# Kernel optimization log

Hardware: AMD Instinct MI355X
Metric: run time of the kernel (lower is better)

## Reference

```python
import jax, jax.numpy as jnp
import numpy as np

N_NODES = 100000
N_EDGES = 600000
DIM = 128
N_BEHAVIORS = 4


def setup_inputs() -> dict:
    key = jax.random.key(0)
    ks = jax.random.split(key, 10)
    user = jax.random.randint(ks[0], (N_NODES,), 0, N_NODES, dtype=jnp.int32)
    item = jax.random.randint(ks[1], (N_NODES,), 0, N_NODES, dtype=jnp.int32)
    behavior = jax.random.randint(ks[2], (N_NODES,), 0, N_BEHAVIORS, dtype=jnp.int32)
    adj_rows = jax.random.randint(ks[3], (N_EDGES,), 0, N_NODES, dtype=jnp.int32)
    adj_cols = jax.random.randint(ks[4], (N_EDGES,), 0, N_NODES, dtype=jnp.int32)
    adj_vals = jax.random.uniform(ks[5], (N_EDGES,), dtype=jnp.float32)
    user_table = jax.random.normal(ks[6], (N_NODES, DIM), dtype=jnp.float32)
    item_table = jax.random.normal(ks[7], (N_NODES, DIM), dtype=jnp.float32)
    behavior_table = jax.random.normal(ks[8], (N_BEHAVIORS, DIM), dtype=jnp.float32)
    kw, kb = jax.random.split(ks[9])
    bound = 1.0 / np.sqrt(DIM)
    W = jax.random.uniform(kw, (DIM, DIM), minval=-bound, maxval=bound, dtype=jnp.float32)
    b = jax.random.uniform(kb, (DIM,), minval=-bound, maxval=bound, dtype=jnp.float32)
    return {"user": user, "item": item, "behavior": behavior,
            "adj_rows": adj_rows, "adj_cols": adj_cols, "adj_vals": adj_vals,
            "user_table": user_table, "item_table": item_table,
            "behavior_table": behavior_table, "W": W, "b": b}


def reference(user, item, behavior, adj_rows, adj_cols, adj_vals,
              user_table, item_table, behavior_table, W, b):
    # embedding sum: [N, D]
    x = user_table[user] + item_table[item] + behavior_table[behavior]
    # sparse adjacency matmul: out[r] = sum_e adj_vals[e] * x[cols[e]] for rows[e]==r
    msg = adj_vals[:, None] * x[adj_cols]                       # [E, D]
    agg = jax.ops.segment_sum(msg, adj_rows, num_segments=N_NODES)  # [N, D]
    # dense linear
    return agg @ W.T + b
```

## Files before the change

### kernel.cpp

```cpp
#include <hip/hip_runtime.h>

#define N_NODES 100000
#define N_EDGES 600000
#define DIM 128

#define N4 (N_NODES / 4)
#define SCAN_BLOCKS ((N_NODES + 1023) / 1024)

#define EMBED_B 6250
#define HIST_B  2344
#define WCONV_B 16
#define GEMM_B   782
#define BUCKET_B 2344
#define NTILES   1563

typedef __attribute__((ext_vector_type(8))) short bf16x8;
typedef __attribute__((ext_vector_type(4))) float f32x4;

__device__ __forceinline__ void fma4(float4& acc, float s, const float4 w) {
    acc.x = fmaf(s, w.x, acc.x);
    acc.y = fmaf(s, w.y, acc.y);
    acc.z = fmaf(s, w.z, acc.z);
    acc.w = fmaf(s, w.w, acc.w);
}

__device__ __forceinline__ unsigned short f2bf(float f) {
    union { float f; unsigned int u; } v; v.f = f;
    unsigned int r = v.u + 0x7fffu + ((v.u >> 16) & 1u);
    return (unsigned short)(r >> 16);
}

__device__ __forceinline__ float bf2f(unsigned short u) {
    union { unsigned int i; float f; } v;
    v.i = ((unsigned int)u) << 16;
    return v.f;
}

__global__ __launch_bounds__(256) void k1_kernel(
    const int* __restrict__ user, const int* __restrict__ item, const int* __restrict__ behavior,
    const float* __restrict__ ut, const float* __restrict__ itb, const float* __restrict__ bt,
    const int* __restrict__ rows, const float* __restrict__ W,
    unsigned short* __restrict__ x16, int* __restrict__ cnt, unsigned short* __restrict__ wfrag)
{
    int b = blockIdx.x;
    int t = threadIdx.x;
    if (b < EMBED_B) {
        int gid = b * 256 + t;
        int r = gid >> 4;
        int m = gid & 15;
        int u  = user[r];
        int iv = item[r];
        int bh = behavior[r];
        const float4* ut4 = (const float4*)ut;
        const float4* it4 = (const float4*)itb;
        const float4* bt4 = (const float4*)bt;
        float4 a0 = ut4[(size_t)u  * 32 + 2 * m];
        float4 a1 = ut4[(size_t)u  * 32 + 2 * m + 1];
        float4 c0 = it4[(size_t)iv * 32 + 2 * m];
        float4 c1 = it4[(size_t)iv * 32 + 2 * m + 1];
        float4 d0 = bt4[(size_t)bh * 32 + 2 * m];
        float4 d1 = bt4[(size_t)bh * 32 + 2 * m + 1];
        ushort4 o0, o1;
        o0.x = f2bf(a0.x + c0.x + d0.x);
        o0.y = f2bf(a0.y + c0.y + d0.y);
        o0.z = f2bf(a0.z + c0.z + d0.z);
        o0.w = f2bf(a0.w + c0.w + d0.w);
        o1.x = f2bf(a1.x + c1.x + d1.x);
        o1.y = f2bf(a1.y + c1.y + d1.y);
        o1.z = f2bf(a1.z + c1.z + d1.z);
        o1.w = f2bf(a1.w + c1.w + d1.w);
        unsigned short* xr = x16 + (size_t)r * DIM + 8 * m;
        *(ushort4*)xr       = o0;
        *(ushort4*)(xr + 4) = o1;
    } else if (b < EMBED_B + HIST_B) {
        int e = (b - EMBED_B) * 256 + t;
        if (e < N_EDGES) atomicAdd(&cnt[rows[e]], 1);
    } else {
        int c4 = (b - EMBED_B - HIST_B) * 256 + t;
        if (c4 < 128 * 128 / 4) {
            float4 wv = ((const float4*)W)[c4];
            int i  = c4 >> 5;
            int k0 = (c4 & 31) * 4;
            int slot = (i >> 4) * 4 + (k0 >> 5);
            int lane = ((k0 & 31) >> 3) * 16 + (i & 15);
            ushort4 o;
            o.x = f2bf(wv.x); o.y = f2bf(wv.y); o.z = f2bf(wv.z); o.w = f2bf(wv.w);
            *(ushort4*)&wfrag[slot * 512 + lane * 8 + (k0 & 7)] = o;
        }
    }
}

__global__ __launch_bounds__(256) void scan1_kernel(
    const int* __restrict__ cnt, int* __restrict__ off, int* __restrict__ bsum)
{
    __shared__ int s[256];
    int t = threadIdx.x;
    int b = blockIdx.x;
    int i4 = b * 256 + t;
    int4 c = {0, 0, 0, 0};
    if (i4 < N4) c = ((const int4*)cnt)[i4];
    int tsum = c.x + c.y + c.z + c.w;
    s[t] = tsum;
    __syncthreads();
    for (int d = 1; d < 256; d <<= 1) {
        int v = (t >= d) ? s[t - d] : 0;
        __syncthreads();
        s[t] += v;
        __syncthreads();
    }
    int texcl = s[t] - tsum;
    if (t == 255) bsum[b] = s[255];
    if (i4 < N4) {
        int4 o;
        o.x = texcl;
        o.y = o.x + c.x;
        o.z = o.y + c.y;
        o.w = o.z + c.z;
        ((int4*)off)[i4] = o;
    }
}

__global__ __launch_bounds__(256) void scan3_kernel(
    const int* __restrict__ bsum, int* __restrict__ off, int* __restrict__ cur)
{
    __shared__ int s[256];
    int t = threadIdx.x;
    int b = blockIdx.x;
    s[t] = (t < b && t < SCAN_BLOCKS) ? bsum[t] : 0;
    __syncthreads();
    for (int d = 1; d < 256; d <<= 1) {
        int v = (t >= d) ? s[t - d] : 0;
        __syncthreads();
        s[t] += v;
        __syncthreads();
    }
    int base = s[255];
    int i4 = b * 256 + t;
    if (i4 < N4) {
        int4 o = ((const int4*)off)[i4];
        o.x += base; o.y += base; o.z += base; o.w += base;
        ((int4*)off)[i4] = o;
        ((int4*)cur)[i4] = o;
    }
    if (b == 0 && t == 0) off[N_NODES] = N_EDGES;
}

__global__ __launch_bounds__(256) void k4_kernel(
    const unsigned short* __restrict__ wfrag, unsigned short* xy,
    const int* __restrict__ rows, const int* __restrict__ cols, const float* __restrict__ vals,
    int* __restrict__ cur, int2* __restrict__ epack)
{
    __shared__ unsigned short wl[128 * 128];
    int b = blockIdx.x;
    int t = threadIdx.x;
    if (b < GEMM_B) {
        for (int i = t; i < 2048; i += 256)
            ((float4*)wl)[i] = ((const float4*)wfrag)[i];
        __syncthreads();

        int l = t & 63;
        int w = t >> 6;
        int c = l & 15;
        int g = l >> 4;
        const bf16x8* wf = (const bf16x8*)wl;

        for (int bt = b; bt < NTILES; bt += GEMM_B) {
            int row = bt * 64 + w * 16 + c;
            int rowc = row < N_NODES ? row : N_NODES - 1;
            const bf16x8* xr = (const bf16x8*)(xy + (size_t)rowc * DIM);
            bf16x8 bfrag[4];
            #pragma unroll
            for (int s = 0; s < 4; ++s) bfrag[s] = xr[g + 4 * s];

            f32x4 acc[8];
            #pragma unroll
            for (int ti = 0; ti < 8; ++ti) acc[ti] = (f32x4){0.f, 0.f, 0.f, 0.f};

            #pragma unroll
            for (int ti = 0; ti < 8; ++ti) {
                #pragma unroll
                for (int s = 0; s < 4; ++s) {
                    bf16x8 af = wf[(ti * 4 + s) * 64 + l];
                    acc[ti] = __builtin_amdgcn_mfma_f32_16x16x32_bf16(af, bfrag[s], acc[ti], 0, 0, 0);
                }
            }

            if (row < N_NODES) {
                unsigned short* yr = xy + (size_t)row * DIM;
                #pragma unroll
                for (int ti = 0; ti < 8; ++ti) {
                    ushort4 o;
                    o.x = f2bf(acc[ti][0]);
                    o.y = f2bf(acc[ti][1]);
                    o.z = f2bf(acc[ti][2]);
                    o.w = f2bf(acc[ti][3]);
                    *(ushort4*)(yr + 16 * ti + 4 * g) = o;
                }
            }
        }
    } else {
        int e = (b - GEMM_B) * 256 + t;
        if (e < N_EDGES) {
            int r = rows[e];
            int slot = atomicAdd(&cur[r], 1);
            int2 p;
            p.x = cols[e];
            p.y = __float_as_int(vals[e]);
            epack[slot] = p;
        }
    }
}

__global__ __launch_bounds__(256) void agg_bias_kernel(
    const int* __restrict__ off, const int2* __restrict__ epack,
    const unsigned short* __restrict__ y, const float* __restrict__ bias,
    float* __restrict__ out)
{
    int gid = blockIdx.x * 256 + threadIdx.x;
    int r = gid >> 4;
    int m = gid & 15;
    if (r >= N_NODES) return;
    int s = off[r], e = off[r + 1];
    const bf16x8* y8 = (const bf16x8*)y;

    float a0[8], a1[8], a2[8], a3[8];
    #pragma unroll
    for (int j = 0; j < 8; ++j) { a0[j] = 0.f; a1[j] = 0.f; a2[j] = 0.f; a3[j] = 0.f; }

    int i = s;
    for (; i + 3 < e; i += 4) {
        int2 p0 = epack[i];
        int2 p1 = epack[i + 1];
        int2 p2 = epack[i + 2];
        int2 p3 = epack[i + 3];
        bf16x8 y0 = y8[(size_t)p0.x * 16 + m];
        bf16x8 y1 = y8[(size_t)p1.x * 16 + m];
        bf16x8 y2 = y8[(size_t)p2.x * 16 + m];
        bf16x8 y3 = y8[(size_t)p3.x * 16 + m];
        float v0 = __int_as_float(p0.y);
        float v1 = __int_as_float(p1.y);
        float v2 = __int_as_float(p2.y);
        float v3 = __int_as_float(p3.y);
        #pragma unroll
        for (int j = 0; j < 8; ++j) {
            a0[j] = fmaf(v0, bf2f((unsigned short)y0[j]), a0[j]);
            a1[j] = fmaf(v1, bf2f((unsigned short)y1[j]), a1[j]);
            a2[j] = fmaf(v2, bf2f((unsigned short)y2[j]), a2[j]);
            a3[j] = fmaf(v3, bf2f((unsigned short)y3[j]), a3[j]);
        }
    }
    for (; i < e; ++i) {
        int2 p0 = epack[i];
        float v0 = __int_as_float(p0.y);
        bf16x8 y0 = y8[(size_t)p0.x * 16 + m];
        #pragma unroll
        for (int j = 0; j < 8; ++j)
            a0[j] = fmaf(v0, bf2f((unsigned short)y0[j]), a0[j]);
    }

    const float4* b4 = (const float4*)bias;
    float4 bb0 = b4[2 * m], bb1 = b4[2 * m + 1];
    float4 o0, o1;
    o0.x = a0[0] + a1[0] + a2[0] + a3[0] + bb0.x;
    o0.y = a0[1] + a1[1] + a2[1] + a3[1] + bb0.y;
    o0.z = a0[2] + a1[2] + a2[2] + a3[2] + bb0.z;
    o0.w = a0[3] + a1[3] + a2[3] + a3[3] + bb0.w;
    o1.x = a0[4] + a1[4] + a2[4] + a3[4] + bb1.x;
    o1.y = a0[5] + a1[5] + a2[5] + a3[5] + bb1.y;
    o1.z = a0[6] + a1[6] + a2[6] + a3[6] + bb1.z;
    o1.w = a0[7] + a1[7] + a2[7] + a3[7] + bb1.w;
    float4* orow = (float4*)(out + (size_t)r * DIM);
    orow[2 * m]     = o0;
    orow[2 * m + 1] = o1;
}


__global__ __launch_bounds__(256) void hist_kernel(
    const int* __restrict__ rows, int* __restrict__ cnt)
{
    int e = blockIdx.x * 256 + threadIdx.x;
    if (e >= N_EDGES) return;
    atomicAdd(&cnt[rows[e]], 1);
}

__global__ __launch_bounds__(256) void bucket_kernel(
    const int* __restrict__ rows, const int* __restrict__ cols, const float* __restrict__ vals,
    int* __restrict__ cur, int2* __restrict__ epack)
{
    int e = blockIdx.x * 256 + threadIdx.x;
    if (e >= N_EDGES) return;
    int r = rows[e];
    int slot = atomicAdd(&cur[r], 1);
    int2 p;
    p.x = cols[e];
    p.y = __float_as_int(vals[e]);
    epack[slot] = p;
}

__global__ __launch_bounds__(256) void agg_fused_kernel(
    const int* __restrict__ off, const int2* __restrict__ epack,
    const int* __restrict__ user, const int* __restrict__ item, const int* __restrict__ behavior,
    const float* __restrict__ ut, const float* __restrict__ itb, const float* __restrict__ bt,
    float* __restrict__ out)
{
    int gid = blockIdx.x * 256 + threadIdx.x;
    int r = gid >> 5;
    int m = gid & 31;
    if (r >= N_NODES) return;
    int s = off[r], e = off[r + 1];
    const float4* ut4 = (const float4*)ut;
    const float4* it4 = (const float4*)itb;
    const float4* bt4 = (const float4*)bt;
    float4 acc = {0.f, 0.f, 0.f, 0.f};
    for (int i = s; i < e; ++i) {
        int2 p = epack[i];
        int c = p.x;
        float v = __int_as_float(p.y);
        float4 a = ut4[(size_t)user[c] * 32 + m];
        float4 cc = it4[(size_t)item[c] * 32 + m];
        float4 d = bt4[(size_t)behavior[c] * 32 + m];
        a.x += cc.x + d.x; a.y += cc.y + d.y; a.z += cc.z + d.z; a.w += cc.w + d.w;
        fma4(acc, v, a);
    }
    ((float4*)out)[(size_t)r * 32 + m] = acc;
}

__global__ __launch_bounds__(256) void scatter_fused_kernel(
    const int* __restrict__ rows, const int* __restrict__ cols, const float* __restrict__ vals,
    const int* __restrict__ user, const int* __restrict__ item, const int* __restrict__ behavior,
    const float* __restrict__ ut, const float* __restrict__ itb, const float* __restrict__ bt,
    float* __restrict__ agg)
{
    int wave = (blockIdx.x * 256 + threadIdx.x) >> 6;
    int lane = threadIdx.x & 63;
    int e = wave * 2 + (lane >> 5);
    if (e >= N_EDGES) return;
    int r = rows[e];
    int c = cols[e];
    float v = vals[e];
    int m = lane & 31;
    const float4* ut4 = (const float4*)ut;
    const float4* it4 = (const float4*)itb;
    const float4* bt4 = (const float4*)bt;
    float4 a = ut4[(size_t)user[c] * 32 + m];
    float4 cc = it4[(size_t)item[c] * 32 + m];
    float4 d = bt4[(size_t)behavior[c] * 32 + m];
    a.x += cc.x + d.x; a.y += cc.y + d.y; a.z += cc.z + d.z; a.w += cc.w + d.w;
    float* o = agg + (size_t)r * DIM + m * 4;
    atomicAdd(o + 0, v * a.x);
    atomicAdd(o + 1, v * a.y);
    atomicAdd(o + 2, v * a.z);
    atomicAdd(o + 3, v * a.w);
}

__global__ __launch_bounds__(256) void gemm_mfma_kernel(
    const float* __restrict__ W, const float* __restrict__ bias, float* io)
{
    __shared__ unsigned short wlds[128 * 128];

    int tid = threadIdx.x;
    for (int c4 = tid; c4 < 128 * 128 / 4; c4 += 256) {
        float4 wv = ((const float4*)W)[c4];
        int i  = c4 >> 5;
        int k0 = (c4 & 31) * 4;
        int slot = (i >> 4) * 4 + (k0 >> 5);
        int lane = ((k0 & 31) >> 3) * 16 + (i & 15);
        ushort4 o;
        o.x = f2bf(wv.x); o.y = f2bf(wv.y); o.z = f2bf(wv.z); o.w = f2bf(wv.w);
        *(ushort4*)&wlds[slot * 512 + lane * 8 + (k0 & 7)] = o;
    }
    __syncthreads();

    int l = tid & 63;
    int w = tid >> 6;
    int c = l & 15;
    int g = l >> 4;
    int row = blockIdx.x * 64 + w * 16 + c;
    int rowc = row < N_NODES ? row : N_NODES - 1;

    const float4* a4 = (const float4*)io;
    bf16x8 bfrag[4];
    #pragma unroll
    for (int s = 0; s < 4; ++s) {
        float4 p0 = a4[(size_t)rowc * 32 + 8 * s + 2 * g];
        float4 p1 = a4[(size_t)rowc * 32 + 8 * s + 2 * g + 1];
        bf16x8 t;
        t[0] = (short)f2bf(p0.x); t[1] = (short)f2bf(p0.y);
        t[2] = (short)f2bf(p0.z); t[3] = (short)f2bf(p0.w);
        t[4] = (short)f2bf(p1.x); t[5] = (short)f2bf(p1.y);
        t[6] = (short)f2bf(p1.z); t[7] = (short)f2bf(p1.w);
        bfrag[s] = t;
    }

    f32x4 acc[8];
    #pragma unroll
    for (int ti = 0; ti < 8; ++ti) acc[ti] = (f32x4){0.f, 0.f, 0.f, 0.f};

    const bf16x8* wf = (const bf16x8*)wlds;
    #pragma unroll
    for (int ti = 0; ti < 8; ++ti) {
        #pragma unroll
        for (int s = 0; s < 4; ++s) {
            bf16x8 af = wf[(ti * 4 + s) * 64 + l];
            acc[ti] = __builtin_amdgcn_mfma_f32_16x16x32_bf16(af, bfrag[s], acc[ti], 0, 0, 0);
        }
    }

    if (row < N_NODES) {
        float4* orow = (float4*)(io + (size_t)row * DIM);
        const float4* b4 = (const float4*)bias;
        #pragma unroll
        for (int ti = 0; ti < 8; ++ti) {
            float4 bb = b4[ti * 4 + g];
            float4 o;
            o.x = acc[ti][0] + bb.x;
            o.y = acc[ti][1] + bb.y;
            o.z = acc[ti][2] + bb.z;
            o.w = acc[ti][3] + bb.w;
            orow[ti * 4 + g] = o;
        }
    }
}

extern "C" void kernel_launch(void* const* d_in, const int* in_sizes, int n_in,
                              void* d_out, int out_size, void* d_ws, size_t ws_size,
                              hipStream_t stream) {
    const int*   user           = (const int*)d_in[0];
    const int*   item           = (const int*)d_in[1];
    const int*   behavior       = (const int*)d_in[2];
    const int*   adj_rows       = (const int*)d_in[3];
    const int*   adj_cols       = (const int*)d_in[4];
    const float* adj_vals       = (const float*)d_in[5];
    const float* user_table     = (const float*)d_in[6];
    const float* item_table     = (const float*)d_in[7];
    const float* behavior_table = (const float*)d_in[8];
    const float* W              = (const float*)d_in[9];
    const float* b              = (const float*)d_in[10];
    float* out = (float*)d_out;

    const size_t X16_BYTES   = (size_t)N_NODES * DIM * sizeof(unsigned short);
    const size_t CNT_BYTES   = (size_t)N_NODES * sizeof(int);
    const size_t OFF_BYTES   = ((size_t)(N_NODES + 1) * sizeof(int) + 15) & ~(size_t)15;
    const size_t EPACK_BYTES = (size_t)N_EDGES * sizeof(int2);
    const size_t WFRAG_BYTES = 128 * 128 * sizeof(unsigned short);

    const int edge_blocks = (N_EDGES + 255) / 256;
    const int agg_blocks  = (N_NODES * 16 + 255) / 256;
    const int gemm_blocks = (N_NODES + 63) / 64;

    char* ws = (char*)d_ws;
    const size_t need_full = X16_BYTES + CNT_BYTES + OFF_BYTES + EPACK_BYTES + WFRAG_BYTES;
    const size_t need_csr  = CNT_BYTES + OFF_BYTES + EPACK_BYTES;

    if (ws_size >= need_full) {
        unsigned short* x16 = (unsigned short*)ws;
        int*  cnt   = (int*)(ws + X16_BYTES);
        int*  off   = (int*)(ws + X16_BYTES + CNT_BYTES);
        int2* epack = (int2*)(ws + X16_BYTES + CNT_BYTES + OFF_BYTES);
        unsigned short* wfrag = (unsigned short*)(ws + X16_BYTES + CNT_BYTES + OFF_BYTES + EPACK_BYTES);
        int*  bsum  = (int*)epack;

        hipMemsetAsync(cnt, 0, CNT_BYTES, stream);
        k1_kernel<<<EMBED_B + HIST_B + WCONV_B, 256, 0, stream>>>(
            user, item, behavior, user_table, item_table, behavior_table,
            adj_rows, W, x16, cnt, wfrag);
        scan1_kernel<<<SCAN_BLOCKS, 256, 0, stream>>>(cnt, off, bsum);
        scan3_kernel<<<SCAN_BLOCKS, 256, 0, stream>>>(bsum, off, cnt);
        k4_kernel<<<GEMM_B + BUCKET_B, 256, 0, stream>>>(
            wfrag, x16, adj_rows, adj_cols, adj_vals, cnt, epack);
        agg_bias_kernel<<<agg_blocks, 256, 0, stream>>>(off, epack, x16, b, out);
    } else if (ws_size >= need_csr) {
        int*  cnt   = (int*)ws;
        int*  off   = (int*)(ws + CNT_BYTES);
        int2* epack = (int2*)(ws + CNT_BYTES + OFF_BYTES);
        int*  bsum  = (int*)epack;

        hipMemsetAsync(cnt, 0, CNT_BYTES, stream);
        hist_kernel<<<edge_blocks, 256, 0, stream>>>(adj_rows, cnt);
        scan1_kernel<<<SCAN_BLOCKS, 256, 0, stream>>>(cnt, off, bsum);
        scan3_kernel<<<SCAN_BLOCKS, 256, 0, stream>>>(bsum, off, cnt);
        bucket_kernel<<<edge_blocks, 256, 0, stream>>>(
            adj_rows, adj_cols, adj_vals, cnt, epack);
        agg_fused_kernel<<<(N_NODES * 32 + 255) / 256, 256, 0, stream>>>(
            off, epack, user, item, behavior,
            user_table, item_table, behavior_table, out);
        gemm_mfma_kernel<<<gemm_blocks, 256, 0, stream>>>(W, b, out);
    } else {
        hipMemsetAsync(d_out, 0, (size_t)N_NODES * DIM * sizeof(float), stream);
        const int scatter_blocks = (N_EDGES / 2 * 64 + 255) / 256;
        scatter_fused_kernel<<<scatter_blocks, 256, 0, stream>>>(
            adj_rows, adj_cols, adj_vals, user, item, behavior,
            user_table, item_table, behavior_table, out);
        gemm_mfma_kernel<<<gemm_blocks, 256, 0, stream>>>(W, b, out);
    }
}
```

Baseline: 137.2 us.

## Two-pass coarse-binned CSR bucketing to localize atomics and scatter writes

Replaces the single-pass edge bucketing (random global atomic per edge plus random scatter) with a two-pass scheme. A new kernel bins edges into 98 coarse row ranges of 1024 rows, using shared-memory counts and one global atomic per bin per block. The placement pass then handles each coarse bin in four chunks, so per-row atomics and epack writes stay within a small address window for better cache locality. The GEMM path now reads W fragments straight from global memory instead of staging them in LDS. This adds an extra temporary buffer and another kernel launch.

```diff
diff --git a/kernel.cpp b/kernel.cpp
--- a/kernel.cpp
+++ b/kernel.cpp
@@ -6,12 +6,15 @@
 
 #define N4 (N_NODES / 4)
 #define SCAN_BLOCKS ((N_NODES + 1023) / 1024)
+#define COARSE 98
 
 #define EMBED_B 6250
 #define HIST_B  2344
 #define WCONV_B 16
+#define BIN_B ((N_EDGES + 1023) / 1024)
 #define GEMM_B   782
-#define BUCKET_B 2344
+#define PLACE_Q  4
+#define PLACE_B  (COARSE * PLACE_Q)
 #define NTILES   1563
 
 typedef __attribute__((ext_vector_type(8))) short bf16x8;
@@ -121,7 +124,8 @@
 }
 
 __global__ __launch_bounds__(256) void scan3_kernel(
-    const int* __restrict__ bsum, int* __restrict__ off, int* __restrict__ cur)
+    const int* __restrict__ bsum, int* __restrict__ off, int* __restrict__ cur,
+    int* __restrict__ coff, int* __restrict__ ccur)
 {
     __shared__ int s[256];
     int t = threadIdx.x;
@@ -142,28 +146,69 @@
         ((int4*)off)[i4] = o;
         ((int4*)cur)[i4] = o;
     }
-    if (b == 0 && t == 0) off[N_NODES] = N_EDGES;
-}
-
-__global__ __launch_bounds__(256) void k4_kernel(
-    const unsigned short* __restrict__ wfrag, unsigned short* xy,
+    if (t == 0) {
+        coff[b] = base;
+        ccur[b] = base;
+        if (b == 0) { off[N_NODES] = N_EDGES; coff[COARSE] = N_EDGES; }
+    }
+}
+
+__global__ __launch_bounds__(256) void bin_kernel(
     const int* __restrict__ rows, const int* __restrict__ cols, const float* __restrict__ vals,
+    int* __restrict__ ccur, int2* __restrict__ tmp)
+{
+    __shared__ int cnt98[128];
+    __shared__ int lcur[128];
+    int b = blockIdx.x;
+    int t = threadIdx.x;
+    if (t < 128) cnt98[t] = 0;
+    __syncthreads();
+    int rr[4], cc[4];
+    float vv[4];
+    int base = b * 1024;
+    #pragma unroll
+    for (int j = 0; j < 4; ++j) {
+        int e = base + t + j * 256;
+        if (e < N_EDGES) {
+            rr[j] = rows[e];
+            cc[j] = cols[e];
+            vv[j] = vals[e];
+            atomicAdd(&cnt98[rr[j] >> 10], 1);
+        } else {
+            rr[j] = -1;
+        }
+    }
+    __syncthreads();
+    if (t < COARSE) {
+        int n = cnt98[t];
+        lcur[t] = n ? atomicAdd(&ccur[t], n) : 0;
+    }
+    __syncthreads();
+    #pragma unroll
+    for (int j = 0; j < 4; ++j) {
+        if (rr[j] >= 0) {
+            int cb = rr[j] >> 10;
+            int dest = atomicAdd(&lcur[cb], 1);
+            int2 pk;
+            pk.x = ((rr[j] & 1023) << 17) | cc[j];
+            pk.y = __float_as_int(vv[j]);
+            tmp[dest] = pk;
+        }
+    }
+}
+
+__global__ __launch_bounds__(256) void k5_kernel(
+    const bf16x8* __restrict__ wf, unsigned short* xy,
+    const int2* __restrict__ tmp, const int* __restrict__ coff,
     int* __restrict__ cur, int2* __restrict__ epack)
 {
-    __shared__ unsigned short wl[128 * 128];
     int b = blockIdx.x;
     int t = threadIdx.x;
     if (b < GEMM_B) {
-        for (int i = t; i < 2048; i += 256)
-            ((float4*)wl)[i] = ((const float4*)wfrag)[i];
-        __syncthreads();
-
         int l = t & 63;
         int w = t >> 6;
         int c = l & 15;
         int g = l >> 4;
-        const bf16x8* wf = (const bf16x8*)wl;
-
         for (int bt = b; bt < NTILES; bt += GEMM_B) {
             int row = bt * 64 + w * 16 + c;
             int rowc = row < N_NODES ? row : N_NODES - 1;
@@ -199,14 +244,22 @@
             }
         }
     } else {
-        int e = (b - GEMM_B) * 256 + t;
-        if (e < N_EDGES) {
-            int r = rows[e];
-            int slot = atomicAdd(&cur[r], 1);
-            int2 p;
-            p.x = cols[e];
-            p.y = __float_as_int(vals[e]);
-            epack[slot] = p;
+        int p = b - GEMM_B;
+        int cb = p >> 2;
+        int q  = p & 3;
+        int s = coff[cb], e = coff[cb + 1];
+        int chunk = (e - s + PLACE_Q - 1) / PLACE_Q;
+        int i0 = s + q * chunk;
+        int i1 = i0 + chunk < e ? i0 + chunk : e;
+        for (int i = i0 + t; i < i1; i += 256) {
+            int2 pk = tmp[i];
+            int row = (cb << 10) | ((unsigned)pk.x >> 17);
+            int col = pk.x & 0x1FFFF;
+            int slot = atomicAdd(&cur[row], 1);
+            int2 o;
+            o.x = col;
+            o.y = pk.y;
+            epack[slot] = o;
         }
     }
 }
@@ -438,26 +491,33 @@
     const float* b              = (const float*)d_in[10];
     float* out = (float*)d_out;
 
-    const size_t X16_BYTES   = (size_t)N_NODES * DIM * sizeof(unsigned short);
-    const size_t CNT_BYTES   = (size_t)N_NODES * sizeof(int);
-    const size_t OFF_BYTES   = ((size_t)(N_NODES + 1) * sizeof(int) + 15) & ~(size_t)15;
-    const size_t EPACK_BYTES = (size_t)N_EDGES * sizeof(int2);
-    const size_t WFRAG_BYTES = 128 * 128 * sizeof(unsigned short);
+    const size_t X16_BYTES    = (size_t)N_NODES * DIM * sizeof(unsigned short);
+    const size_t CNT_BYTES    = (size_t)N_NODES * sizeof(int);
+    const size_t OFF_BYTES    = ((size_t)(N_NODES + 1) * sizeof(int) + 15) & ~(size_t)15;
+    const size_t EPACK_BYTES  = (size_t)N_EDGES * sizeof(int2);
+    const size_t WFRAG_BYTES  = 128 * 128 * sizeof(unsigned short);
+    const size_t TMP_BYTES    = (size_t)N_EDGES * sizeof(int2);
+    const size_t COARSE_BYTES = 1024;
 
     const int edge_blocks = (N_EDGES + 255) / 256;
     const int agg_blocks  = (N_NODES * 16 + 255) / 256;
     const int gemm_blocks = (N_NODES + 63) / 64;
 
     char* ws = (char*)d_ws;
-    const size_t need_full = X16_BYTES + CNT_BYTES + OFF_BYTES + EPACK_BYTES + WFRAG_BYTES;
+    const size_t need_full = X16_BYTES + CNT_BYTES + OFF_BYTES + EPACK_BYTES +
+                             WFRAG_BYTES + TMP_BYTES + COARSE_BYTES;
     const size_t need_csr  = CNT_BYTES + OFF_BYTES + EPACK_BYTES;
 
     if (ws_size >= need_full) {
-        unsigned short* x16 = (unsigned short*)ws;
-        int*  cnt   = (int*)(ws + X16_BYTES);
-        int*  off   = (int*)(ws + X16_BYTES + CNT_BYTES);
-        int2* epack = (int2*)(ws + X16_BYTES + CNT_BYTES + OFF_BYTES);
-        unsigned short* wfrag = (unsigned short*)(ws + X16_BYTES + CNT_BYTES + OFF_BYTES + EPACK_BYTES);
+        size_t o = 0;
+        unsigned short* x16 = (unsigned short*)(ws + o); o += X16_BYTES;
+        int*  cnt   = (int*)(ws + o); o += CNT_BYTES;
+        int*  off   = (int*)(ws + o); o += OFF_BYTES;
+        int2* epack = (int2*)(ws + o); o += EPACK_BYTES;
+        unsigned short* wfrag = (unsigned short*)(ws + o); o += WFRAG_BYTES;
+        int2* tmp   = (int2*)(ws + o); o += TMP_BYTES;
+        int*  coff  = (int*)(ws + o);
+        int*  ccur  = coff + 128;
         int*  bsum  = (int*)epack;
 
         hipMemsetAsync(cnt, 0, CNT_BYTES, stream);
@@ -465,20 +525,25 @@
             user, item, behavior, user_table, item_table, behavior_table,
             adj_rows, W, x16, cnt, wfrag);
         scan1_kernel<<<SCAN_BLOCKS, 256, 0, stream>>>(cnt, off, bsum);
-        scan3_kernel<<<SCAN_BLOCKS, 256, 0, stream>>>(bsum, off, cnt);
-        k4_kernel<<<GEMM_B + BUCKET_B, 256, 0, stream>>>(
-            wfrag, x16, adj_rows, adj_cols, adj_vals, cnt, epack);
+        scan3_kernel<<<SCAN_BLOCKS, 256, 0, stream>>>(bsum, off, cnt, coff, ccur);
+        bin_kernel<<<BIN_B, 256, 0, stream>>>(
+            adj_rows, adj_cols, adj_vals, ccur, tmp);
+        k5_kernel<<<GEMM_B + PLACE_B, 256, 0, stream>>>(
+            (const bf16x8*)wfrag, x16, tmp, coff, cnt, epack);
         agg_bias_kernel<<<agg_blocks, 256, 0, stream>>>(off, epack, x16, b, out);
     } else if (ws_size >= need_csr) {
         int*  cnt   = (int*)ws;
         int*  off   = (int*)(ws + CNT_BYTES);
         int2* epack = (int2*)(ws + CNT_BYTES + OFF_BYTES);
         int*  bsum  = (int*)epack;
+        int   cdummy[2];
+        (void)cdummy;
 
         hipMemsetAsync(cnt, 0, CNT_BYTES, stream);
         hist_kernel<<<edge_blocks, 256, 0, stream>>>(adj_rows, cnt);
         scan1_kernel<<<SCAN_BLOCKS, 256, 0, stream>>>(cnt, off, bsum);
-        scan3_kernel<<<SCAN_BLOCKS, 256, 0, stream>>>(bsum, off, cnt);
+        scan3_kernel<<<SCAN_BLOCKS, 256, 0, stream>>>(bsum, off, cnt,
+            (int*)(epack + N_EDGES - 256), (int*)(epack + N_EDGES - 128));
         bucket_kernel<<<edge_blocks, 256, 0, stream>>>(
             adj_rows, adj_cols, adj_vals, cnt, epack);
         agg_fused_kernel<<<(N_NODES * 32 + 255) / 256, 256, 0, stream>>>(
```

Result: slower. 143.7 us (+4.8%).

## Software-pipeline embedding gather across rows and read GEMM weights directly from global

Applied to the files above, without the earlier changes.

The embedding stage now gives each thread group four rows strided by 25000 and prefetches the next row's table entries while converting and storing the current one, which cuts the block count and hides gather latency. The GEMM part of k4 no longer stages W fragments in shared memory and no longer loops over tiles. It launches one block per 64-row tile and reads the bf16 fragments straight from global memory, relying on L1/L2 caching. This removes the LDS fill and barrier, but every wave now loads the 32KB of weights from cache, and the prefetch adds register pressure.

```diff
diff --git a/kernel.cpp b/kernel.cpp
--- a/kernel.cpp
+++ b/kernel.cpp
@@ -7,12 +7,12 @@
 #define N4 (N_NODES / 4)
 #define SCAN_BLOCKS ((N_NODES + 1023) / 1024)
 
-#define EMBED_B 6250
+#define EMBED_B 1563
 #define HIST_B  2344
 #define WCONV_B 16
-#define GEMM_B   782
+#define NGROUP  25000
+#define GEMM_B   1563
 #define BUCKET_B 2344
-#define NTILES   1563
 
 typedef __attribute__((ext_vector_type(8))) short bf16x8;
 typedef __attribute__((ext_vector_type(4))) float f32x4;
@@ -46,32 +46,49 @@
     int t = threadIdx.x;
     if (b < EMBED_B) {
         int gid = b * 256 + t;
-        int r = gid >> 4;
+        int g = gid >> 4;
         int m = gid & 15;
-        int u  = user[r];
-        int iv = item[r];
-        int bh = behavior[r];
-        const float4* ut4 = (const float4*)ut;
-        const float4* it4 = (const float4*)itb;
-        const float4* bt4 = (const float4*)bt;
-        float4 a0 = ut4[(size_t)u  * 32 + 2 * m];
-        float4 a1 = ut4[(size_t)u  * 32 + 2 * m + 1];
-        float4 c0 = it4[(size_t)iv * 32 + 2 * m];
-        float4 c1 = it4[(size_t)iv * 32 + 2 * m + 1];
-        float4 d0 = bt4[(size_t)bh * 32 + 2 * m];
-        float4 d1 = bt4[(size_t)bh * 32 + 2 * m + 1];
-        ushort4 o0, o1;
-        o0.x = f2bf(a0.x + c0.x + d0.x);
-        o0.y = f2bf(a0.y + c0.y + d0.y);
-        o0.z = f2bf(a0.z + c0.z + d0.z);
-        o0.w = f2bf(a0.w + c0.w + d0.w);
-        o1.x = f2bf(a1.x + c1.x + d1.x);
-        o1.y = f2bf(a1.y + c1.y + d1.y);
-        o1.z = f2bf(a1.z + c1.z + d1.z);
-        o1.w = f2bf(a1.w + c1.w + d1.w);
-        unsigned short* xr = x16 + (size_t)r * DIM + 8 * m;
-        *(ushort4*)xr       = o0;
-        *(ushort4*)(xr + 4) = o1;
+        if (g < NGROUP) {
+            const float4* ut4 = (const float4*)ut;
+            const float4* it4 = (const float4*)itb;
+            const float4* bt4 = (const float4*)bt;
+            int r = g;
+            int u = user[r], iv = item[r], bh = behavior[r];
+            float4 a0 = ut4[(size_t)u  * 32 + 2 * m];
+            float4 a1 = ut4[(size_t)u  * 32 + 2 * m + 1];
+            float4 c0 = it4[(size_t)iv * 32 + 2 * m];
+            float4 c1 = it4[(size_t)iv * 32 + 2 * m + 1];
+            float4 d0 = bt4[(size_t)bh * 32 + 2 * m];
+            float4 d1 = bt4[(size_t)bh * 32 + 2 * m + 1];
+            #pragma unroll
+            for (int k = 0; k < 4; ++k) {
+                float4 na0, na1, nc0, nc1, nd0, nd1;
+                int rn = r + NGROUP;
+                if (k < 3) {
+                    int un = user[rn], ivn = item[rn], bhn = behavior[rn];
+                    na0 = ut4[(size_t)un  * 32 + 2 * m];
+                    na1 = ut4[(size_t)un  * 32 + 2 * m + 1];
+                    nc0 = it4[(size_t)ivn * 32 + 2 * m];
+                    nc1 = it4[(size_t)ivn * 32 + 2 * m + 1];
+                    nd0 = bt4[(size_t)bhn * 32 + 2 * m];
+                    nd1 = bt4[(size_t)bhn * 32 + 2 * m + 1];
+                }
+                ushort4 o0, o1;
+                o0.x = f2bf(a0.x + c0.x + d0.x);
+                o0.y = f2bf(a0.y + c0.y + d0.y);
+                o0.z = f2bf(a0.z + c0.z + d0.z);
+                o0.w = f2bf(a0.w + c0.w + d0.w);
+                o1.x = f2bf(a1.x + c1.x + d1.x);
+                o1.y = f2bf(a1.y + c1.y + d1.y);
+                o1.z = f2bf(a1.z + c1.z + d1.z);
+                o1.w = f2bf(a1.w + c1.w + d1.w);
+                unsigned short* xr = x16 + (size_t)r * DIM + 8 * m;
+                *(ushort4*)xr       = o0;
+                *(ushort4*)(xr + 4) = o1;
+                r = rn;
+                a0 = na0; a1 = na1; c0 = nc0; c1 = nc1; d0 = nd0; d1 = nd1;
+            }
+        }
     } else if (b < EMBED_B + HIST_B) {
         int e = (b - EMBED_B) * 256 + t;
         if (e < N_EDGES) atomicAdd(&cnt[rows[e]], 1);
@@ -146,56 +163,47 @@
 }
 
 __global__ __launch_bounds__(256) void k4_kernel(
-    const unsigned short* __restrict__ wfrag, unsigned short* xy,
+    const bf16x8* __restrict__ wf, unsigned short* xy,
     const int* __restrict__ rows, const int* __restrict__ cols, const float* __restrict__ vals,
     int* __restrict__ cur, int2* __restrict__ epack)
 {
-    __shared__ unsigned short wl[128 * 128];
     int b = blockIdx.x;
     int t = threadIdx.x;
     if (b < GEMM_B) {
-        for (int i = t; i < 2048; i += 256)
-            ((float4*)wl)[i] = ((const float4*)wfrag)[i];
-        __syncthreads();
-
         int l = t & 63;
         int w = t >> 6;
         int c = l & 15;
         int g = l >> 4;
-        const bf16x8* wf = (const bf16x8*)wl;
-
-        for (int bt = b; bt < NTILES; bt += GEMM_B) {
-            int row = bt * 64 + w * 16 + c;
-            int rowc = row < N_NODES ? row : N_NODES - 1;
-            const bf16x8* xr = (const bf16x8*)(xy + (size_t)rowc * DIM);
-            bf16x8 bfrag[4];
+        int row = b * 64 + w * 16 + c;
+        int rowc = row < N_NODES ? row : N_NODES - 1;
+        const bf16x8* xr = (const bf16x8*)(xy + (size_t)rowc * DIM);
+        bf16x8 bfrag[4];
+        #pragma unroll
+        for (int s = 0; s < 4; ++s) bfrag[s] = xr[g + 4 * s];
+
+        f32x4 acc[8];
+        #pragma unroll
+        for (int ti = 0; ti < 8; ++ti) acc[ti] = (f32x4){0.f, 0.f, 0.f, 0.f};
+
+        #pragma unroll
+        for (int ti = 0; ti < 8; ++ti) {
             #pragma unroll
-            for (int s = 0; s < 4; ++s) bfrag[s] = xr[g + 4 * s];
-
-            f32x4 acc[8];
-            #pragma unroll
-            for (int ti = 0; ti < 8; ++ti) acc[ti] = (f32x4){0.f, 0.f, 0.f, 0.f};
-
+            for (int s = 0; s < 4; ++s) {
+                bf16x8 af = wf[(ti * 4 + s) * 64 + l];
+                acc[ti] = __builtin_amdgcn_mfma_f32_16x16x32_bf16(af, bfrag[s], acc[ti], 0, 0, 0);
+            }
+        }
+
+        if (row < N_NODES) {
+            unsigned short* yr = xy + (size_t)row * DIM;
             #pragma unroll
             for (int ti = 0; ti < 8; ++ti) {
-                #pragma unroll
-                for (int s = 0; s < 4; ++s) {
-                    bf16x8 af = wf[(ti * 4 + s) * 64 + l];
-                    acc[ti] = __builtin_amdgcn_mfma_f32_16x16x32_bf16(af, bfrag[s], acc[ti], 0, 0, 0);
-                }
-            }
-
-            if (row < N_NODES) {
-                unsigned short* yr = xy + (size_t)row * DIM;
-                #pragma unroll
-                for (int ti = 0; ti < 8; ++ti) {
-                    ushort4 o;
-                    o.x = f2bf(acc[ti][0]);
-                    o.y = f2bf(acc[ti][1]);
-                    o.z = f2bf(acc[ti][2]);
-                    o.w = f2bf(acc[ti][3]);
-                    *(ushort4*)(yr + 16 * ti + 4 * g) = o;
-                }
+                ushort4 o;
+                o.x = f2bf(acc[ti][0]);
+                o.y = f2bf(acc[ti][1]);
+                o.z = f2bf(acc[ti][2]);
+                o.w = f2bf(acc[ti][3]);
+                *(ushort4*)(yr + 16 * ti + 4 * g) = o;
             }
         }
     } else {
@@ -453,11 +461,12 @@
     const size_t need_csr  = CNT_BYTES + OFF_BYTES + EPACK_BYTES;
 
     if (ws_size >= need_full) {
-        unsigned short* x16 = (unsigned short*)ws;
-        int*  cnt   = (int*)(ws + X16_BYTES);
-        int*  off   = (int*)(ws + X16_BYTES + CNT_BYTES);
-        int2* epack = (int2*)(ws + X16_BYTES + CNT_BYTES + OFF_BYTES);
-        unsigned short* wfrag = (unsigned short*)(ws + X16_BYTES + CNT_BYTES + OFF_BYTES + EPACK_BYTES);
+        size_t o = 0;
+        unsigned short* x16 = (unsigned short*)(ws + o); o += X16_BYTES;
+        int*  cnt   = (int*)(ws + o); o += CNT_BYTES;
+        int*  off   = (int*)(ws + o); o += OFF_BYTES;
+        int2* epack = (int2*)(ws + o); o += EPACK_BYTES;
+        unsigned short* wfrag = (unsigned short*)(ws + o);
         int*  bsum  = (int*)epack;
 
         hipMemsetAsync(cnt, 0, CNT_BYTES, stream);
@@ -467,7 +476,7 @@
         scan1_kernel<<<SCAN_BLOCKS, 256, 0, stream>>>(cnt, off, bsum);
         scan3_kernel<<<SCAN_BLOCKS, 256, 0, stream>>>(bsum, off, cnt);
         k4_kernel<<<GEMM_B + BUCKET_B, 256, 0, stream>>>(
-            wfrag, x16, adj_rows, adj_cols, adj_vals, cnt, epack);
+            (const bf16x8*)wfrag, x16, adj_rows, adj_cols, adj_vals, cnt, epack);
         agg_bias_kernel<<<agg_blocks, 256, 0, stream>>>(off, epack, x16, b, out);
     } else if (ws_size >= need_csr) {
         int*  cnt   = (int*)ws;
```

Result: no change. 139.6 us (+1.8%).

## Fuse embedding gather into MFMA GEMM, dropping the bf16 x intermediate

Applied to the files above, without the earlier changes.

The embedding sum is no longer written to a bf16 x buffer in the first kernel. The GEMM blocks now gather user, item and behavior rows, sum them, pack them straight into MFMA B fragments and write y. This removes a 25.6MB write and re-read of x and shortens the first kernel to just the histogram and W conversion. As a trade-off, W fragments are now read from global/L2 instead of LDS, one tile per block with no persistent loop, so GEMM blocks may stall on scattered table gathers while the bucket blocks run alongside them.

```diff
diff --git a/kernel.cpp b/kernel.cpp
--- a/kernel.cpp
+++ b/kernel.cpp
@@ -7,12 +7,10 @@
 #define N4 (N_NODES / 4)
 #define SCAN_BLOCKS ((N_NODES + 1023) / 1024)
 
-#define EMBED_B 6250
 #define HIST_B  2344
 #define WCONV_B 16
-#define GEMM_B   782
 #define BUCKET_B 2344
-#define NTILES   1563
+#define FUSED_B  1563
 
 typedef __attribute__((ext_vector_type(8))) short bf16x8;
 typedef __attribute__((ext_vector_type(4))) float f32x4;
@@ -36,47 +34,17 @@
     return v.f;
 }
 
-__global__ __launch_bounds__(256) void k1_kernel(
-    const int* __restrict__ user, const int* __restrict__ item, const int* __restrict__ behavior,
-    const float* __restrict__ ut, const float* __restrict__ itb, const float* __restrict__ bt,
-    const int* __restrict__ rows, const float* __restrict__ W,
-    unsigned short* __restrict__ x16, int* __restrict__ cnt, unsigned short* __restrict__ wfrag)
+__global__ __launch_bounds__(256) void hw_kernel(
+    const int* __restrict__ rows, int* __restrict__ cnt,
+    const float* __restrict__ W, unsigned short* __restrict__ wfrag)
 {
     int b = blockIdx.x;
     int t = threadIdx.x;
-    if (b < EMBED_B) {
-        int gid = b * 256 + t;
-        int r = gid >> 4;
-        int m = gid & 15;
-        int u  = user[r];
-        int iv = item[r];
-        int bh = behavior[r];
-        const float4* ut4 = (const float4*)ut;
-        const float4* it4 = (const float4*)itb;
-        const float4* bt4 = (const float4*)bt;
-        float4 a0 = ut4[(size_t)u  * 32 + 2 * m];
-        float4 a1 = ut4[(size_t)u  * 32 + 2 * m + 1];
-        float4 c0 = it4[(size_t)iv * 32 + 2 * m];
-        float4 c1 = it4[(size_t)iv * 32 + 2 * m + 1];
-        float4 d0 = bt4[(size_t)bh * 32 + 2 * m];
-        float4 d1 = bt4[(size_t)bh * 32 + 2 * m + 1];
-        ushort4 o0, o1;
-        o0.x = f2bf(a0.x + c0.x + d0.x);
-        o0.y = f2bf(a0.y + c0.y + d0.y);
-        o0.z = f2bf(a0.z + c0.z + d0.z);
-        o0.w = f2bf(a0.w + c0.w + d0.w);
-        o1.x = f2bf(a1.x + c1.x + d1.x);
-        o1.y = f2bf(a1.y + c1.y + d1.y);
-        o1.z = f2bf(a1.z + c1.z + d1.z);
-        o1.w = f2bf(a1.w + c1.w + d1.w);
-        unsigned short* xr = x16 + (size_t)r * DIM + 8 * m;
-        *(ushort4*)xr       = o0;
-        *(ushort4*)(xr + 4) = o1;
-    } else if (b < EMBED_B + HIST_B) {
-        int e = (b - EMBED_B) * 256 + t;
+    if (b < HIST_B) {
+        int e = b * 256 + t;
         if (e < N_EDGES) atomicAdd(&cnt[rows[e]], 1);
     } else {
-        int c4 = (b - EMBED_B - HIST_B) * 256 + t;
+        int c4 = (b - HIST_B) * 256 + t;
         if (c4 < 128 * 128 / 4) {
             float4 wv = ((const float4*)W)[c4];
             int i  = c4 >> 5;
@@ -145,61 +113,17 @@
     if (b == 0 && t == 0) off[N_NODES] = N_EDGES;
 }
 
-__global__ __launch_bounds__(256) void k4_kernel(
-    const unsigned short* __restrict__ wfrag, unsigned short* xy,
+__global__ __launch_bounds__(256) void kb_kernel(
     const int* __restrict__ rows, const int* __restrict__ cols, const float* __restrict__ vals,
-    int* __restrict__ cur, int2* __restrict__ epack)
-{
-    __shared__ unsigned short wl[128 * 128];
+    int* __restrict__ cur, int2* __restrict__ epack,
+    const int* __restrict__ user, const int* __restrict__ item, const int* __restrict__ behavior,
+    const float* __restrict__ ut, const float* __restrict__ itb, const float* __restrict__ bt,
+    const bf16x8* __restrict__ wf, unsigned short* __restrict__ y)
+{
     int b = blockIdx.x;
     int t = threadIdx.x;
-    if (b < GEMM_B) {
-        for (int i = t; i < 2048; i += 256)
-            ((float4*)wl)[i] = ((const float4*)wfrag)[i];
-        __syncthreads();
-
-        int l = t & 63;
-        int w = t >> 6;
-        int c = l & 15;
-        int g = l >> 4;
-        const bf16x8* wf = (const bf16x8*)wl;
-
-        for (int bt = b; bt < NTILES; bt += GEMM_B) {
-            int row = bt * 64 + w * 16 + c;
-            int rowc = row < N_NODES ? row : N_NODES - 1;
-            const bf16x8* xr = (const bf16x8*)(xy + (size_t)rowc * DIM);
-            bf16x8 bfrag[4];
-            #pragma unroll
-            for (int s = 0; s < 4; ++s) bfrag[s] = xr[g + 4 * s];
-
-            f32x4 acc[8];
-            #pragma unroll
-            for (int ti = 0; ti < 8; ++ti) acc[ti] = (f32x4){0.f, 0.f, 0.f, 0.f};
-
-            #pragma unroll
-            for (int ti = 0; ti < 8; ++ti) {
-                #pragma unroll
-                for (int s = 0; s < 4; ++s) {
-                    bf16x8 af = wf[(ti * 4 + s) * 64 + l];
-                    acc[ti] = __builtin_amdgcn_mfma_f32_16x16x32_bf16(af, bfrag[s], acc[ti], 0, 0, 0);
-                }
-            }
-
-            if (row < N_NODES) {
-                unsigned short* yr = xy + (size_t)row * DIM;
-                #pragma unroll
-                for (int ti = 0; ti < 8; ++ti) {
-                    ushort4 o;
-                    o.x = f2bf(acc[ti][0]);
-                    o.y = f2bf(acc[ti][1]);
-                    o.z = f2bf(acc[ti][2]);
-                    o.w = f2bf(acc[ti][3]);
-                    *(ushort4*)(yr + 16 * ti + 4 * g) = o;
-                }
-            }
-        }
-    } else {
-        int e = (b - GEMM_B) * 256 + t;
+    if (b < BUCKET_B) {
+        int e = b * 256 + t;
         if (e < N_EDGES) {
             int r = rows[e];
             int slot = atomicAdd(&cur[r], 1);
@@ -207,6 +131,69 @@
             p.x = cols[e];
             p.y = __float_as_int(vals[e]);
             epack[slot] = p;
+        }
+    } else {
+        int b2 = b - BUCKET_B;
+        int l = t & 63;
+        int w = t >> 6;
+        int c = l & 15;
+        int g = l >> 4;
+        int row = b2 * 64 + w * 16 + c;
+        int rowc = row < N_NODES ? row : N_NODES - 1;
+
+        int u  = user[rowc];
+        int iv = item[rowc];
+        int bh = behavior[rowc];
+        const float4* ut4 = (const float4*)ut;
+        const float4* it4 = (const float4*)itb;
+        const float4* bt4 = (const float4*)bt;
+
+        bf16x8 bfrag[4];
+        #pragma unroll
+        for (int s = 0; s < 4; ++s) {
+            int base = 8 * s + 2 * g;
+            float4 a0 = ut4[(size_t)u  * 32 + base];
+            float4 a1 = ut4[(size_t)u  * 32 + base + 1];
+            float4 c0 = it4[(size_t)iv * 32 + base];
+            float4 c1 = it4[(size_t)iv * 32 + base + 1];
+            float4 d0 = bt4[(size_t)bh * 32 + base];
+            float4 d1 = bt4[(size_t)bh * 32 + base + 1];
+            bf16x8 tt;
+            tt[0] = (short)f2bf(a0.x + c0.x + d0.x);
+            tt[1] = (short)f2bf(a0.y + c0.y + d0.y);
+            tt[2] = (short)f2bf(a0.z + c0.z + d0.z);
+            tt[3] = (short)f2bf(a0.w + c0.w + d0.w);
+            tt[4] = (short)f2bf(a1.x + c1.x + d1.x);
+            tt[5] = (short)f2bf(a1.y + c1.y + d1.y);
+            tt[6] = (short)f2bf(a1.z + c1.z + d1.z);
+            tt[7] = (short)f2bf(a1.w + c1.w + d1.w);
+            bfrag[s] = tt;
+        }
+
+        f32x4 acc[8];
+        #pragma unroll
+        for (int ti = 0; ti < 8; ++ti) acc[ti] = (f32x4){0.f, 0.f, 0.f, 0.f};
+
+        #pragma unroll
+        for (int ti = 0; ti < 8; ++ti) {
+            #pragma unroll
+            for (int s = 0; s < 4; ++s) {
+                bf16x8 af = wf[(ti * 4 + s) * 64 + l];
+                acc[ti] = __builtin_amdgcn_mfma_f32_16x16x32_bf16(af, bfrag[s], acc[ti], 0, 0, 0);
+            }
+        }
+
+        if (row < N_NODES) {
+            unsigned short* yr = y + (size_t)row * DIM;
+            #pragma unroll
+            for (int ti = 0; ti < 8; ++ti) {
+                ushort4 o;
+                o.x = f2bf(acc[ti][0]);
+                o.y = f2bf(acc[ti][1]);
+                o.z = f2bf(acc[ti][2]);
+                o.w = f2bf(acc[ti][3]);
+                *(ushort4*)(yr + 16 * ti + 4 * g) = o;
+            }
         }
     }
 }
@@ -438,7 +425,7 @@
     const float* b              = (const float*)d_in[10];
     float* out = (float*)d_out;
 
-    const size_t X16_BYTES   = (size_t)N_NODES * DIM * sizeof(unsigned short);
+    const size_t Y_BYTES     = (size_t)N_NODES * DIM * sizeof(unsigned short);
     const size_t CNT_BYTES   = (size_t)N_NODES * sizeof(int);
     const size_t OFF_BYTES   = ((size_t)(N_NODES + 1) * sizeof(int) + 15) & ~(size_t)15;
     const size_t EPACK_BYTES = (size_t)N_EDGES * sizeof(int2);
@@ -449,26 +436,27 @@
     const int gemm_blocks = (N_NODES + 63) / 64;
 
     char* ws = (char*)d_ws;
-    const size_t need_full = X16_BYTES + CNT_BYTES + OFF_BYTES + EPACK_BYTES + WFRAG_BYTES;
+    const size_t need_full = Y_BYTES + CNT_BYTES + OFF_BYTES + EPACK_BYTES + WFRAG_BYTES;
     const size_t need_csr  = CNT_BYTES + OFF_BYTES + EPACK_BYTES;
 
     if (ws_size >= need_full) {
-        unsigned short* x16 = (unsigned short*)ws;
-        int*  cnt   = (int*)(ws + X16_BYTES);
-        int*  off   = (int*)(ws + X16_BYTES + CNT_BYTES);
-        int2* epack = (int2*)(ws + X16_BYTES + CNT_BYTES + OFF_BYTES);
-        unsigned short* wfrag = (unsigned short*)(ws + X16_BYTES + CNT_BYTES + OFF_BYTES + EPACK_BYTES);
+        size_t o = 0;
+        unsigned short* y = (unsigned short*)(ws + o); o += Y_BYTES;
+        int*  cnt   = (int*)(ws + o); o += CNT_BYTES;
+        int*  off   = (int*)(ws + o); o += OFF_BYTES;
+        int2* epack = (int2*)(ws + o); o += EPACK_BYTES;
+        unsigned short* wfrag = (unsigned short*)(ws + o);
         int*  bsum  = (int*)epack;
 
         hipMemsetAsync(cnt, 0, CNT_BYTES, stream);
-        k1_kernel<<<EMBED_B + HIST_B + WCONV_B, 256, 0, stream>>>(
-            user, item, behavior, user_table, item_table, behavior_table,
-            adj_rows, W, x16, cnt, wfrag);
+        hw_kernel<<<HIST_B + WCONV_B, 256, 0, stream>>>(adj_rows, cnt, W, wfrag);
         scan1_kernel<<<SCAN_BLOCKS, 256, 0, stream>>>(cnt, off, bsum);
         scan3_kernel<<<SCAN_BLOCKS, 256, 0, stream>>>(bsum, off, cnt);
-        k4_kernel<<<GEMM_B + BUCKET_B, 256, 0, stream>>>(
-            wfrag, x16, adj_rows, adj_cols, adj_vals, cnt, epack);
-        agg_bias_kernel<<<agg_blocks, 256, 0, stream>>>(off, epack, x16, b, out);
+        kb_kernel<<<BUCKET_B + FUSED_B, 256, 0, stream>>>(
+            adj_rows, adj_cols, adj_vals, cnt, epack,
+            user, item, behavior, user_table, item_table, behavior_table,
+            (const bf16x8*)wfrag, y);
+        agg_bias_kernel<<<agg_blocks, 256, 0, stream>>>(off, epack, y, b, out);
     } else if (ws_size >= need_csr) {
         int*  cnt   = (int*)ws;
         int*  off   = (int*)(ws + CNT_BYTES);
```

New measurement: 155.0 us. 1.13x slower.
